# Optimization experiments

Measured on AMD Instinct MI355X. Metric: run time of the kernel, lower is better.

## Reference

```python
import jax, jax.numpy as jnp
import numpy as np
import math

D_MODEL = 512


def setup_inputs() -> dict:
    key = jax.random.key(0)
    x = jax.random.normal(key, (16384, 32), dtype=jnp.float32)
    return {"x": x}


def reference(x) -> jnp.ndarray:
    # x: [B, F]; output: [B, D_MODEL]
    d_model = D_MODEL
    # div_term: [D/2]
    div_term = jnp.exp(jnp.arange(0, d_model, 2, dtype=jnp.float32) * (-(math.log(10000.0) / d_model)))
    # sinusoid input: [B, F, D/2]
    si = x[:, :, None] * div_term
    sin_mean = jnp.sin(si).mean(axis=1)  # [B, D/2]
    cos_mean = jnp.cos(si).mean(axis=1)  # [B, D/2]
    # interleave: out[:, 0::2] = sin_mean, out[:, 1::2] = cos_mean
    out = jnp.stack([sin_mean, cos_mean], axis=-1).reshape(x.shape[0], d_model)
    return out
```

## Files before the change

kernel.cpp:

```cpp
#include <hip/hip_runtime.h>

#define F 32
#define D_HALF 256
#define NP 14
#define TPB 256
#define BLOCKS 2048

__device__ constexpr float kTable[NP] = {
     3.125e-2f,
    -1.5625e-2f,
    -5.2083333333333e-3f,
     1.3020833333333e-3f,
     2.6041666666667e-4f,
    -4.3402777777778e-5f,
    -6.2003968253968e-6f,
     7.7504960317460e-7f,
     8.6116622574956e-8f,
    -8.6116622574956e-9f,
    -7.8287838704505e-10f,
     6.5239865587088e-11f,
     5.0184511989929e-12f,
    -3.5846079992806e-13f
};

__global__ __launch_bounds__(TPB) void pe_kernel(const float* __restrict__ x,
                                                 float4* __restrict__ out,
                                                 int B) {
    const int lane = threadIdx.x & 63;
    const int fl   = lane & 31;
    const int half = lane >> 5;
    const int gwave  = blockIdx.x * (TPB / 64) + (threadIdx.x >> 6);
    const int nwaves = gridDim.x * (TPB / 64);
    const int npairs = B >> 1;

    const float kExp = -0.05190512648261503f;

    float d0[4], t0[4], d1[4], t1[4];
#pragma unroll
    for (int m = 0; m < 4; ++m) {
        const int j0 = 2 * fl + 64 * m;
        d0[m] = __builtin_amdgcn_exp2f((float)j0 * kExp);
        d1[m] = __builtin_amdgcn_exp2f((float)(j0 + 1) * kExp);
        t0[m] = d0[m] * d0[m];
        t1[m] = d1[m] * d1[m];
    }

    for (int rp = gwave; rp < npairs; rp += nwaves) {
        const int r = (rp << 1) + half;
        const float v = x[r * F + fl];

        float mom[NP];
        float p = v;
#pragma unroll
        for (int k = 0; k < NP; ++k) { mom[k] = p; p *= v; }
#pragma unroll
        for (int k = 0; k < NP; ++k) {
            float s = mom[k];
            s += __shfl_xor(s, 1);
            s += __shfl_xor(s, 2);
            s += __shfl_xor(s, 4);
            s += __shfl_xor(s, 8);
            s += __shfl_xor(s, 16);
            mom[k] = s * kTable[k];
        }

        float4* orow = out + r * (D_HALF / 2);
#pragma unroll
        for (int m = 0; m < 4; ++m) {
            float s0 = mom[12];
            s0 = fmaf(s0, t0[m], mom[10]);
            s0 = fmaf(s0, t0[m], mom[8]);
            s0 = fmaf(s0, t0[m], mom[6]);
            s0 = fmaf(s0, t0[m], mom[4]);
            s0 = fmaf(s0, t0[m], mom[2]);
            s0 = fmaf(s0, t0[m], mom[0]);
            float c0 = mom[13];
            c0 = fmaf(c0, t0[m], mom[11]);
            c0 = fmaf(c0, t0[m], mom[9]);
            c0 = fmaf(c0, t0[m], mom[7]);
            c0 = fmaf(c0, t0[m], mom[5]);
            c0 = fmaf(c0, t0[m], mom[3]);
            c0 = fmaf(c0, t0[m], mom[1]);
            c0 = fmaf(c0, t0[m], 1.0f);

            float s1 = mom[12];
            s1 = fmaf(s1, t1[m], mom[10]);
            s1 = fmaf(s1, t1[m], mom[8]);
            s1 = fmaf(s1, t1[m], mom[6]);
            s1 = fmaf(s1, t1[m], mom[4]);
            s1 = fmaf(s1, t1[m], mom[2]);
            s1 = fmaf(s1, t1[m], mom[0]);
            float c1 = mom[13];
            c1 = fmaf(c1, t1[m], mom[11]);
            c1 = fmaf(c1, t1[m], mom[9]);
            c1 = fmaf(c1, t1[m], mom[7]);
            c1 = fmaf(c1, t1[m], mom[5]);
            c1 = fmaf(c1, t1[m], mom[3]);
            c1 = fmaf(c1, t1[m], mom[1]);
            c1 = fmaf(c1, t1[m], 1.0f);

            orow[fl + 32 * m] = make_float4(s0 * d0[m], c0, s1 * d1[m], c1);
        }
    }
}

extern "C" void kernel_launch(void* const* d_in, const int* in_sizes, int n_in,
                              void* d_out, int out_size, void* d_ws, size_t ws_size,
                              hipStream_t stream) {
    const float* x = (const float*)d_in[0];
    float4* out = (float4*)d_out;
    const int B = in_sizes[0] / F;
    pe_kernel<<<BLOCKS, TPB, 0, stream>>>(x, out, B);
}
```

Before: 68.78 us.

## Process one row per wave with split moment halves and DPP reductions

Each wave now handles a single row. The two 32-lane halves compute the low seven and high seven power moments (the upper half uses a base of v^8), which halves the per-lane moment work. Cross-lane sums use DPP row operations plus a row_bcast, and readlane broadcasts the totals into scalars. This replaces 70 shuffles with 35 DPP adds and 14 readlanes. The output loop now covers 64 lanes by 2 blocks, using the fact that div_term for column j+64 is 0.01 times div_term for column j, which saves exp calls. The cost is rounding drift from the v^8 factoring and a reliance on the DPP broadcast semantics.

```diff
diff --git a/kernel.cpp b/kernel.cpp
--- a/kernel.cpp
+++ b/kernel.cpp
@@ -1,12 +1,10 @@
 #include <hip/hip_runtime.h>
 
 #define F 32
-#define D_HALF 256
-#define NP 14
 #define TPB 256
 #define BLOCKS 2048
 
-__device__ constexpr float kTable[NP] = {
+__device__ constexpr float kTable[14] = {
      3.125e-2f,
     -1.5625e-2f,
     -5.2083333333333e-3f,
@@ -23,83 +21,95 @@
     -3.5846079992806e-13f
 };
 
+#define DPP_ADD(x, ctrl)                                                                 \
+    x += __int_as_float(__builtin_amdgcn_update_dpp(                                     \
+        0, __float_as_int(x), (ctrl), 0xf, 0xf, true))
+
+#define RDLANE(x, l) __int_as_float(__builtin_amdgcn_readlane(__float_as_int(x), (l)))
+
 __global__ __launch_bounds__(TPB) void pe_kernel(const float* __restrict__ x,
                                                  float4* __restrict__ out,
                                                  int B) {
     const int lane = threadIdx.x & 63;
     const int fl   = lane & 31;
-    const int half = lane >> 5;
+    const bool hi  = lane >= 32;
     const int gwave  = blockIdx.x * (TPB / 64) + (threadIdx.x >> 6);
     const int nwaves = gridDim.x * (TPB / 64);
-    const int npairs = B >> 1;
 
     const float kExp = -0.05190512648261503f;
 
-    float d0[4], t0[4], d1[4], t1[4];
+    float coef[7];
 #pragma unroll
-    for (int m = 0; m < 4; ++m) {
-        const int j0 = 2 * fl + 64 * m;
-        d0[m] = __builtin_amdgcn_exp2f((float)j0 * kExp);
-        d1[m] = __builtin_amdgcn_exp2f((float)(j0 + 1) * kExp);
-        t0[m] = d0[m] * d0[m];
-        t1[m] = d1[m] * d1[m];
-    }
+    for (int k = 0; k < 7; ++k) coef[k] = hi ? kTable[7 + k] : kTable[k];
 
-    for (int rp = gwave; rp < npairs; rp += nwaves) {
-        const int r = (rp << 1) + half;
+    float d[4], t[4];
+    d[0] = __builtin_amdgcn_exp2f((float)(2 * lane) * kExp);
+    d[1] = __builtin_amdgcn_exp2f((float)(2 * lane + 1) * kExp);
+    d[2] = d[0] * 0.01f;
+    d[3] = d[1] * 0.01f;
+#pragma unroll
+    for (int m = 0; m < 4; ++m) t[m] = d[m] * d[m];
+
+    for (int r = gwave; r < B; r += nwaves) {
         const float v = x[r * F + fl];
+        const float v2 = v * v,   v3 = v2 * v,  v4 = v2 * v2,
+                    v5 = v3 * v2, v6 = v3 * v3, v8 = v4 * v4;
+        const float base = hi ? v8 : v;
 
-        float mom[NP];
-        float p = v;
+        float rm[7];
+        rm[0] = base * coef[0];
+        rm[1] = (base * coef[1]) * v;
+        rm[2] = (base * coef[2]) * v2;
+        rm[3] = (base * coef[3]) * v3;
+        rm[4] = (base * coef[4]) * v4;
+        rm[5] = (base * coef[5]) * v5;
+        rm[6] = (base * coef[6]) * v6;
+
 #pragma unroll
-        for (int k = 0; k < NP; ++k) { mom[k] = p; p *= v; }
-#pragma unroll
-        for (int k = 0; k < NP; ++k) {
-            float s = mom[k];
-            s += __shfl_xor(s, 1);
-            s += __shfl_xor(s, 2);
-            s += __shfl_xor(s, 4);
-            s += __shfl_xor(s, 8);
-            s += __shfl_xor(s, 16);
-            mom[k] = s * kTable[k];
+        for (int k = 0; k < 7; ++k) {
+            DPP_ADD(rm[k], 0x111);
+            DPP_ADD(rm[k], 0x112);
+            DPP_ADD(rm[k], 0x114);
+            DPP_ADD(rm[k], 0x118);
+            DPP_ADD(rm[k], 0x142);
         }
 
-        float4* orow = out + r * (D_HALF / 2);
+        const float M1  = RDLANE(rm[0], 31), M2  = RDLANE(rm[1], 31),
+                    M3  = RDLANE(rm[2], 31), M4  = RDLANE(rm[3], 31),
+                    M5  = RDLANE(rm[4], 31), M6  = RDLANE(rm[5], 31),
+                    M7  = RDLANE(rm[6], 31),
+                    M8  = RDLANE(rm[0], 63), M9  = RDLANE(rm[1], 63),
+                    M10 = RDLANE(rm[2], 63), M11 = RDLANE(rm[3], 63),
+                    M12 = RDLANE(rm[4], 63), M13 = RDLANE(rm[5], 63),
+                    M14 = RDLANE(rm[6], 63);
+
+        float4* orow = out + r * (512 / 4);
 #pragma unroll
-        for (int m = 0; m < 4; ++m) {
-            float s0 = mom[12];
-            s0 = fmaf(s0, t0[m], mom[10]);
-            s0 = fmaf(s0, t0[m], mom[8]);
-            s0 = fmaf(s0, t0[m], mom[6]);
-            s0 = fmaf(s0, t0[m], mom[4]);
-            s0 = fmaf(s0, t0[m], mom[2]);
-            s0 = fmaf(s0, t0[m], mom[0]);
-            float c0 = mom[13];
-            c0 = fmaf(c0, t0[m], mom[11]);
-            c0 = fmaf(c0, t0[m], mom[9]);
-            c0 = fmaf(c0, t0[m], mom[7]);
-            c0 = fmaf(c0, t0[m], mom[5]);
-            c0 = fmaf(c0, t0[m], mom[3]);
-            c0 = fmaf(c0, t0[m], mom[1]);
-            c0 = fmaf(c0, t0[m], 1.0f);
+        for (int m = 0; m < 2; ++m) {
+            const float ta = t[2 * m], tb = t[2 * m + 1];
 
-            float s1 = mom[12];
-            s1 = fmaf(s1, t1[m], mom[10]);
-            s1 = fmaf(s1, t1[m], mom[8]);
-            s1 = fmaf(s1, t1[m], mom[6]);
-            s1 = fmaf(s1, t1[m], mom[4]);
-            s1 = fmaf(s1, t1[m], mom[2]);
-            s1 = fmaf(s1, t1[m], mom[0]);
-            float c1 = mom[13];
-            c1 = fmaf(c1, t1[m], mom[11]);
-            c1 = fmaf(c1, t1[m], mom[9]);
-            c1 = fmaf(c1, t1[m], mom[7]);
-            c1 = fmaf(c1, t1[m], mom[5]);
-            c1 = fmaf(c1, t1[m], mom[3]);
-            c1 = fmaf(c1, t1[m], mom[1]);
-            c1 = fmaf(c1, t1[m], 1.0f);
+            float s0 = M13;
+            s0 = fmaf(s0, ta, M11); s0 = fmaf(s0, ta, M9);
+            s0 = fmaf(s0, ta, M7);  s0 = fmaf(s0, ta, M5);
+            s0 = fmaf(s0, ta, M3);  s0 = fmaf(s0, ta, M1);
+            float c0 = M14;
+            c0 = fmaf(c0, ta, M12); c0 = fmaf(c0, ta, M10);
+            c0 = fmaf(c0, ta, M8);  c0 = fmaf(c0, ta, M6);
+            c0 = fmaf(c0, ta, M4);  c0 = fmaf(c0, ta, M2);
+            c0 = fmaf(c0, ta, 1.0f);
 
-            orow[fl + 32 * m] = make_float4(s0 * d0[m], c0, s1 * d1[m], c1);
+            float s1 = M13;
+            s1 = fmaf(s1, tb, M11); s1 = fmaf(s1, tb, M9);
+            s1 = fmaf(s1, tb, M7);  s1 = fmaf(s1, tb, M5);
+            s1 = fmaf(s1, tb, M3);  s1 = fmaf(s1, tb, M1);
+            float c1 = M14;
+            c1 = fmaf(c1, tb, M12); c1 = fmaf(c1, tb, M10);
+            c1 = fmaf(c1, tb, M8);  c1 = fmaf(c1, tb, M6);
+            c1 = fmaf(c1, tb, M4);  c1 = fmaf(c1, tb, M2);
+            c1 = fmaf(c1, tb, 1.0f);
+
+            orow[lane + 64 * m] =
+                make_float4(s0 * d[2 * m], c0, s1 * d[2 * m + 1], c1);
         }
     }
 }
```

After: 66.05 us. -4.0%, faster.
